# Kernel tuning notes

Hardware: AMD Instinct MI355X
Metric: run time of the kernel (lower is better)

## Reference

```python
import jax, jax.numpy as jnp
from jax import lax
import numpy as np

# Vim-tiny config
D_MODEL, D_INNER, D_STATE, DT_RANK, K_CONV, DEPTH = 192, 384, 16, 12, 4, 24
BATCH, IMG, PATCH = 8, 224, 16
L = (IMG // PATCH) ** 2  # 196 tokens
EPS = 1e-5


def setup_inputs() -> dict:
    key = jax.random.key(0)
    ks = jax.random.split(key, 12)
    std = 0.02
    x = jax.random.normal(ks[0], (BATCH, 3, IMG, IMG), jnp.float32)
    patch_w = jax.random.normal(ks[1], (D_MODEL, 3, PATCH, PATCH), jnp.float32) * std
    patch_b = jnp.zeros((D_MODEL,), jnp.float32)
    norm_w = jnp.ones((DEPTH, D_MODEL), jnp.float32)
    norm_b = jnp.zeros((DEPTH, D_MODEL), jnp.float32)
    in_proj_w = jax.random.normal(ks[2], (DEPTH, 2 * D_INNER, D_MODEL), jnp.float32) * std
    conv_w = jax.random.normal(ks[3], (DEPTH, D_INNER, K_CONV), jnp.float32) * 0.2
    conv_b = jnp.zeros((DEPTH, D_INNER), jnp.float32)
    x_proj_w = jax.random.normal(ks[4], (DEPTH, DT_RANK + 2 * D_STATE, D_INNER), jnp.float32) * std
    dt_proj_w = jax.random.normal(ks[5], (DEPTH, D_INNER, DT_RANK), jnp.float32) * std
    # softplus^{-1}(0.01): standard mamba dt init
    dt_proj_b = jnp.full((DEPTH, D_INNER), float(np.log(np.expm1(0.01))), jnp.float32)
    # S4D-real init: A = -[1..d_state]
    A_log = jnp.broadcast_to(jnp.log(jnp.arange(1, D_STATE + 1, dtype=jnp.float32)),
                             (DEPTH, D_INNER, D_STATE)).copy()
    D_param = jnp.ones((DEPTH, D_INNER), jnp.float32)
    out_proj_w = jax.random.normal(ks[6], (DEPTH, D_MODEL, D_INNER), jnp.float32) * std
    normf_w = jnp.ones((D_MODEL,), jnp.float32)
    normf_b = jnp.zeros((D_MODEL,), jnp.float32)
    return dict(x=x, patch_w=patch_w, patch_b=patch_b, norm_w=norm_w, norm_b=norm_b,
                in_proj_w=in_proj_w, conv_w=conv_w, conv_b=conv_b, x_proj_w=x_proj_w,
                dt_proj_w=dt_proj_w, dt_proj_b=dt_proj_b, A_log=A_log, D_param=D_param,
                out_proj_w=out_proj_w, normf_w=normf_w, normf_b=normf_b)


def layernorm(h, w, b):
    mu = jnp.mean(h, axis=-1, keepdims=True)
    var = jnp.mean(jnp.square(h - mu), axis=-1, keepdims=True)
    return (h - mu) * lax.rsqrt(var + EPS) * w + b


def mamba_mixer(h, ipw, cw, cb, xpw, dtw, dtb, a_log, d_p, opw):
    # h: [B, L, d_model]
    xz = jnp.einsum('bld,ed->ble', h, ipw)          # [B, L, 2*d_inner]
    xi, z = jnp.split(xz, 2, axis=-1)
    # depthwise causal conv1d (left pad k-1, keep first L outputs)
    xt = xi.transpose(0, 2, 1)                       # [B, d_inner, L]
    xc = lax.conv_general_dilated(xt, cw[:, None, :], (1,), [(K_CONV - 1, 0)],
                                  dimension_numbers=('NCH', 'OIH', 'NCH'),
                                  feature_group_count=D_INNER) + cb[None, :, None]
    xc = jax.nn.silu(xc).transpose(0, 2, 1)          # [B, L, d_inner]
    dbl = jnp.einsum('bld,ed->ble', xc, xpw)         # [B, L, dt_rank+2*d_state]
    dt = jax.nn.softplus(jnp.einsum('blr,dr->bld', dbl[..., :DT_RANK], dtw) + dtb)
    Bm = dbl[..., DT_RANK:DT_RANK + D_STATE]         # [B, L, d_state]
    Cm = dbl[..., DT_RANK + D_STATE:]                # [B, L, d_state]
    A = -jnp.exp(a_log)                              # [d_inner, d_state]
    dA = jnp.exp(dt[..., None] * A)                  # [B, L, d_inner, d_state]
    dBx = (dt * xc)[..., None] * Bm[:, :, None, :]   # [B, L, d_inner, d_state]

    def step(hst, inp):
        a, bx, c = inp
        hst = a * hst + bx
        return hst, jnp.einsum('bds,bs->bd', hst, c)

    h0 = jnp.zeros((h.shape[0], D_INNER, D_STATE), h.dtype)
    _, ys = lax.scan(step, h0, (dA.transpose(1, 0, 2, 3), dBx.transpose(1, 0, 2, 3),
                                Cm.transpose(1, 0, 2)))
    y = ys.transpose(1, 0, 2) + d_p * xc             # [B, L, d_inner]
    y = y * jax.nn.silu(z)
    return jnp.einsum('ble,de->bld', y, opw)


def reference(x, patch_w, patch_b, norm_w, norm_b, in_proj_w, conv_w, conv_b,
              x_proj_w, dt_proj_w, dt_proj_b, A_log, D_param, out_proj_w,
              normf_w, normf_b):
    # patch embedding: strided conv then flatten HW -> tokens
    emb = lax.conv_general_dilated(x, patch_w, (PATCH, PATCH), 'VALID',
                                   dimension_numbers=('NCHW', 'OIHW', 'NCHW'))
    emb = emb + patch_b[None, :, None, None]
    b = emb.shape[0]
    hidden = emb.reshape(b, D_MODEL, -1).transpose(0, 2, 1)   # [B, L, d_model]
    residual = jnp.zeros_like(hidden)

    def layer_step(carry, p):
        h, res = carry
        nw, nb, ipw, cw, cb, xpw, dtw, dtb, al, dp, opw = p
        res = res + h
        h = layernorm(res, nw, nb)
        h = mamba_mixer(h, ipw, cw, cb, xpw, dtw, dtb, al, dp, opw)
        return (h, res), None

    (hidden, residual), _ = lax.scan(
        layer_step, (hidden, residual),
        (norm_w, norm_b, in_proj_w, conv_w, conv_b, x_proj_w,
         dt_proj_w, dt_proj_b, A_log, D_param, out_proj_w))
    residual = residual + hidden
    return layernorm(residual, normf_w, normf_b)     # [B, L, d_model]
```

## Files before the change

kernel.cpp:

```cpp
#include <hip/hip_runtime.h>

#define NROWS 1568
#define MPAD  1600
#define LSEQ  196
#define EPS   1e-5f
#define TCH   7
#define NCH   28

typedef __attribute__((ext_vector_type(8))) short short8_t;
typedef __attribute__((ext_vector_type(8))) unsigned short ush8;
typedef __attribute__((ext_vector_type(4))) float f32x4;
typedef unsigned short ush;

__device__ __forceinline__ float silu_(float x) { return x / (1.f + expf(-x)); }
__device__ __forceinline__ float fsilu_(float x) { return x / (1.f + __expf(-x)); }

__device__ __forceinline__ ush bfh_(float f) {
  unsigned u = __float_as_uint(f);
  return (ush)((u + 0x7FFFu + ((u >> 16) & 1u)) >> 16);
}
__device__ __forceinline__ float bf2f_(ush h) {
  return __uint_as_float(((unsigned)h) << 16);
}

__device__ __forceinline__ void glds16(const ush* g, ush* l) {
  __builtin_amdgcn_global_load_lds(
      (const __attribute__((address_space(1))) void*)g,
      (__attribute__((address_space(3))) void*)l, 16, 0, 0);
}

#define N8_PW  18432
#define N8_IPW 442368
#define N8_OPW 221184
__global__ __launch_bounds__(256) void wsplit3_k(const float* __restrict__ pw,
                                                 const float* __restrict__ ipw,
                                                 const float* __restrict__ opw,
                                                 ush* __restrict__ pw_h, ush* __restrict__ pw_l,
                                                 ush* __restrict__ ipw_h, ush* __restrict__ ipw_l,
                                                 ush* __restrict__ opw_h, ush* __restrict__ opw_l) {
  int i = blockIdx.x * 256 + threadIdx.x;
  const float* src;
  ush *hi, *lo;
  size_t off;
  if (i < N8_PW) { src = pw; hi = pw_h; lo = pw_l; off = i; }
  else if (i < N8_PW + N8_IPW) { src = ipw; hi = ipw_h; lo = ipw_l; off = i - N8_PW; }
  else if (i < N8_PW + N8_IPW + N8_OPW) { src = opw; hi = opw_h; lo = opw_l; off = i - N8_PW - N8_IPW; }
  else return;
  float v[8];
  *(float4*)&v[0] = *(const float4*)(src + off * 8);
  *(float4*)&v[4] = *(const float4*)(src + off * 8 + 4);
  ush8 h8, l8;
#pragma unroll
  for (int j = 0; j < 8; ++j) {
    ush h = bfh_(v[j]);
    h8[j] = h;
    l8[j] = bfh_(v[j] - bf2f_(h));
  }
  *(ush8*)&hi[off * 8] = h8;
  *(ush8*)&lo[off * 8] = l8;
}

__global__ __launch_bounds__(256) void zeros_k(float* __restrict__ res,
                                               ush* __restrict__ a_h, ush* __restrict__ a_l,
                                               ush* __restrict__ hn_h, ush* __restrict__ hn_l,
                                               ush* __restrict__ y_h, ush* __restrict__ y_l) {
  int i = blockIdx.x * 256 + threadIdx.x;
  ush8 z = {};
  if (i < 75264) ((float4*)res)[i] = float4{0.f, 0.f, 0.f, 0.f};
  if (i < 3072) {
    ((ush8*)(a_h + (size_t)NROWS * 768))[i] = z;
    ((ush8*)(a_l + (size_t)NROWS * 768))[i] = z;
  }
  if (i < 768) {
    ((ush8*)(hn_h + (size_t)NROWS * 192))[i] = z;
    ((ush8*)(hn_l + (size_t)NROWS * 192))[i] = z;
  }
  if (i < 1536) {
    ((ush8*)(y_h + (size_t)NROWS * 384))[i] = z;
    ((ush8*)(y_l + (size_t)NROWS * 384))[i] = z;
  }
}

__global__ __launch_bounds__(256) void im2col_k(const float* __restrict__ x,
                                                ush* __restrict__ Ah,
                                                ush* __restrict__ Al) {
  int i8 = blockIdx.x * 256 + threadIdx.x;
  if (i8 >= NROWS * 768 / 8) return;
  int idx = i8 * 8;
  int m = idx / 768, r = idx - m * 768;
  int b = m / LSEQ, l = m - b * LSEQ;
  int ph = l / 14, pw = l - ph * 14;
  int c = r >> 8, rem = r & 255, ii = rem >> 4, j = rem & 15;
  const float* src = &x[((b * 3 + c) * 224 + ph * 16 + ii) * 224 + pw * 16 + j];
  float v[8];
  *(float4*)&v[0] = *(const float4*)&src[0];
  *(float4*)&v[4] = *(const float4*)&src[4];
  ush8 h8, l8;
#pragma unroll
  for (int k = 0; k < 8; ++k) {
    ush h = bfh_(v[k]);
    h8[k] = h;
    l8[k] = bfh_(v[k] - bf2f_(h));
  }
  *(ush8*)&Ah[idx] = h8;
  *(ush8*)&Al[idx] = l8;
}

__global__ __launch_bounds__(256) void gemm64g_k(const ush* __restrict__ Ah_g,
                                                 const ush* __restrict__ Al_g,
                                                 const ush* __restrict__ Wh_g,
                                                 const ush* __restrict__ Wl_g,
                                                 const float* __restrict__ bias,
                                                 float* __restrict__ C, int N, int K) {
  __shared__ ush sAh[3][2048], sAl[3][2048], sWh[3][2048], sWl[3][2048];
  const int tid = threadIdx.x, lane = tid & 63, wave = tid >> 6;
  const int ntiles = N / 64;
  const int row0 = (blockIdx.x / ntiles) * 64, col0 = (blockIdx.x % ntiles) * 64;
  const int sr = wave * 16 + (lane >> 2);
  const int j8 = ((lane & 3) ^ ((sr >> 1) & 3)) * 8;
  const size_t gaA = (size_t)(row0 + sr) * K + j8;
  const size_t gaW = (size_t)(col0 + sr) * K + j8;
  const int lb = wave * 512;
  const int nsteps = K >> 5;

  glds16(Ah_g + gaA, &sAh[0][lb]);
  glds16(Al_g + gaA, &sAl[0][lb]);
  glds16(Wh_g + gaW, &sWh[0][lb]);
  glds16(Wl_g + gaW, &sWl[0][lb]);
  glds16(Ah_g + gaA + 32, &sAh[1][lb]);
  glds16(Al_g + gaA + 32, &sAl[1][lb]);
  glds16(Wh_g + gaW + 32, &sWh[1][lb]);
  glds16(Wl_g + gaW + 32, &sWl[1][lb]);

  const int fr = lane & 15, fg = lane >> 4;
  const int wm = (wave & 1) * 32, wn = (wave >> 1) * 32;
  f32x4 acc[2][2] = {};
  int cur = 0;

  for (int s = 0; s < nsteps; ++s) {
    if (s < nsteps - 1) asm volatile("s_waitcnt vmcnt(4)" ::: "memory");
    else                asm volatile("s_waitcnt vmcnt(0)" ::: "memory");
    __builtin_amdgcn_s_barrier();
    __builtin_amdgcn_sched_barrier(0);
    if (s + 2 < nsteps) {
      int nk = (s + 2) * 32;
      int nb = (cur >= 1) ? cur - 1 : 2;
      glds16(Ah_g + gaA + nk, &sAh[nb][lb]);
      glds16(Al_g + gaA + nk, &sAl[nb][lb]);
      glds16(Wh_g + gaW + nk, &sWh[nb][lb]);
      glds16(Wl_g + gaW + nk, &sWl[nb][lb]);
    }
    short8_t ah[2], al[2], wh[2], wl[2];
#pragma unroll
    for (int i = 0; i < 2; ++i) {
      int ra = wm + i * 16 + fr;
      int oa = ra * 32 + ((fg ^ ((ra >> 1) & 3)) << 3);
      ah[i] = *(short8_t*)&sAh[cur][oa];
      al[i] = *(short8_t*)&sAl[cur][oa];
      int rw = wn + i * 16 + fr;
      int ow = rw * 32 + ((fg ^ ((rw >> 1) & 3)) << 3);
      wh[i] = *(short8_t*)&sWh[cur][ow];
      wl[i] = *(short8_t*)&sWl[cur][ow];
    }
#pragma unroll
    for (int i = 0; i < 2; ++i)
#pragma unroll
      for (int j = 0; j < 2; ++j) {
        acc[i][j] = __builtin_amdgcn_mfma_f32_16x16x32_bf16(ah[i], wh[j], acc[i][j], 0, 0, 0);
        acc[i][j] = __builtin_amdgcn_mfma_f32_16x16x32_bf16(ah[i], wl[j], acc[i][j], 0, 0, 0);
        acc[i][j] = __builtin_amdgcn_mfma_f32_16x16x32_bf16(al[i], wh[j], acc[i][j], 0, 0, 0);
      }
    cur = (cur == 2) ? 0 : cur + 1;
  }

#pragma unroll
  for (int i = 0; i < 2; ++i)
#pragma unroll
    for (int j = 0; j < 2; ++j)
#pragma unroll
      for (int r = 0; r < 4; ++r) {
        int m = row0 + wm + i * 16 + fg * 4 + r;
        int n = col0 + wn + j * 16 + fr;
        float o = acc[i][j][r];
        if (bias) o += bias[n];
        C[(size_t)m * N + n] = o;
      }
}

__global__ __launch_bounds__(256) void gemm32g_k(const ush* __restrict__ Ah_g,
                                                 const ush* __restrict__ Al_g,
                                                 const ush* __restrict__ Wh_g,
                                                 const ush* __restrict__ Wl_g,
                                                 float* __restrict__ C, int N, int K) {
  __shared__ ush sAh[3][1024], sAl[3][1024], sWh[3][1024], sWl[3][1024];
  const int tid = threadIdx.x, lane = tid & 63, wave = tid >> 6;
  const int ntiles = N / 32;
  const int row0 = (blockIdx.x / ntiles) * 32, col0 = (blockIdx.x % ntiles) * 32;
  const int sr = (wave & 1) * 16 + (lane >> 2);
  const int j8 = ((lane & 3) ^ ((sr >> 1) & 3)) * 8;
  const bool isA = wave < 2;
  const size_t ga = (size_t)((isA ? row0 : col0) + sr) * K + j8;
  const ush* gh = isA ? Ah_g : Wh_g;
  const ush* gl = isA ? Al_g : Wl_g;
  const int lb = (wave & 1) * 512;
  const int nsteps = K >> 5;

  {
    ush* dh0 = isA ? &sAh[0][lb] : &sWh[0][lb];
    ush* dl0 = isA ? &sAl[0][lb] : &sWl[0][lb];
    glds16(gh + ga, dh0);
    glds16(gl + ga, dl0);
    ush* dh1 = isA ? &sAh[1][lb] : &sWh[1][lb];
    ush* dl1 = isA ? &sAl[1][lb] : &sWl[1][lb];
    glds16(gh + ga + 32, dh1);
    glds16(gl + ga + 32, dl1);
  }

  const int fr = lane & 15, fg = lane >> 4;
  const int wrow = wave & 1, wcol = wave >> 1;
  f32x4 acc = {};
  int cur = 0;

  for (int s = 0; s < nsteps; ++s) {
    if (s < nsteps - 1) asm volatile("s_waitcnt vmcnt(2)" ::: "memory");
    else                asm volatile("s_waitcnt vmcnt(0)" ::: "memory");
    __builtin_amdgcn_s_barrier();
    __builtin_amdgcn_sched_barrier(0);
    if (s + 2 < nsteps) {
      int nk = (s + 2) * 32;
      int nb = (cur >= 1) ? cur - 1 : 2;
      ush* dh = isA ? &sAh[nb][lb] : &sWh[nb][lb];
      ush* dl = isA ? &sAl[nb][lb] : &sWl[nb][lb];
      glds16(gh + ga + nk, dh);
      glds16(gl + ga + nk, dl);
    }
    int ra = wrow * 16 + fr;
    int oa = ra * 32 + ((fg ^ ((ra >> 1) & 3)) << 3);
    short8_t ah = *(short8_t*)&sAh[cur][oa];
    short8_t al = *(short8_t*)&sAl[cur][oa];
    int rw = wcol * 16 + fr;
    int ow = rw * 32 + ((fg ^ ((rw >> 1) & 3)) << 3);
    short8_t wh = *(short8_t*)&sWh[cur][ow];
    short8_t wl = *(short8_t*)&sWl[cur][ow];
    acc = __builtin_amdgcn_mfma_f32_16x16x32_bf16(ah, wh, acc, 0, 0, 0);
    acc = __builtin_amdgcn_mfma_f32_16x16x32_bf16(ah, wl, acc, 0, 0, 0);
    acc = __builtin_amdgcn_mfma_f32_16x16x32_bf16(al, wh, acc, 0, 0, 0);
    cur = (cur == 2) ? 0 : cur + 1;
  }

#pragma unroll
  for (int r = 0; r < 4; ++r) {
    int m = row0 + wrow * 16 + fg * 4 + r;
    int n = col0 + wcol * 16 + fr;
    C[(size_t)m * N + n] = acc[r];
  }
}

__global__ __launch_bounds__(256) void addlnbf_k(float* __restrict__ res,
                                                 const float* __restrict__ h,
                                                 const float* __restrict__ w,
                                                 const float* __restrict__ b,
                                                 ush* __restrict__ out_h,
                                                 ush* __restrict__ out_l) {
  int n = blockIdx.x * 4 + (threadIdx.x >> 6);
  int t = threadIdx.x & 63;
  float v[3];
  float s = 0.f;
#pragma unroll
  for (int i = 0; i < 3; ++i) {
    int d = t + 64 * i;
    float r = res[(size_t)n * 192 + d] + h[(size_t)n * 192 + d];
    res[(size_t)n * 192 + d] = r;
    v[i] = r;
    s += r;
  }
#pragma unroll
  for (int off = 32; off >= 1; off >>= 1) s += __shfl_xor(s, off);
  float mu = s * (1.f / 192.f);
  float q = 0.f;
#pragma unroll
  for (int i = 0; i < 3; ++i) { float dd = v[i] - mu; q += dd * dd; }
#pragma unroll
  for (int off = 32; off >= 1; off >>= 1) q += __shfl_xor(q, off);
  float inv = rsqrtf(q * (1.f / 192.f) + EPS);
#pragma unroll
  for (int i = 0; i < 3; ++i) {
    int d = t + 64 * i;
    float o = (v[i] - mu) * inv * w[d] + b[d];
    ush hh = bfh_(o);
    out_h[(size_t)n * 192 + d] = hh;
    out_l[(size_t)n * 192 + d] = bfh_(o - bf2f_(hh));
  }
}

__global__ __launch_bounds__(256) void lnfin_k(const float* __restrict__ res,
                                               const float* __restrict__ h,
                                               const float* __restrict__ w,
                                               const float* __restrict__ b,
                                               float* __restrict__ out) {
  int n = blockIdx.x * 4 + (threadIdx.x >> 6);
  int lane = threadIdx.x & 63;
  if (n >= NROWS) return;
  float v[3];
  float s = 0.f;
#pragma unroll
  for (int i = 0; i < 3; ++i) {
    int d = lane + 64 * i;
    float r = res[(size_t)n * 192 + d] + h[(size_t)n * 192 + d];
    v[i] = r;
    s += r;
  }
#pragma unroll
  for (int off = 32; off >= 1; off >>= 1) s += __shfl_xor(s, off);
  float mu = s * (1.f / 192.f);
  float q = 0.f;
#pragma unroll
  for (int i = 0; i < 3; ++i) { float dd = v[i] - mu; q += dd * dd; }
#pragma unroll
  for (int off = 32; off >= 1; off >>= 1) q += __shfl_xor(q, off);
  float inv = rsqrtf(q * (1.f / 192.f) + EPS);
#pragma unroll
  for (int i = 0; i < 3; ++i) {
    int d = lane + 64 * i;
    out[(size_t)n * 192 + d] = (v[i] - mu) * inv * w[d] + b[d];
  }
}

__global__ __launch_bounds__(384) void conv4_k(const float* __restrict__ xz,
                                               const float* __restrict__ cw,
                                               const float* __restrict__ cb,
                                               const float* __restrict__ xpw,
                                               const float* __restrict__ dtw,
                                               const float* __restrict__ dtb,
                                               const float* __restrict__ dpar,
                                               float* __restrict__ dbl,
                                               float* __restrict__ pk) {
  __shared__ __align__(16) float xcl[4][384];
  __shared__ __align__(16) float dbll[4][48];
  const int t = threadIdx.x;
  const int n0 = blockIdx.x * 4;
  const int l0 = n0 % LSEQ;

  float cwv[4];
  *(float4*)cwv = *(const float4*)(cw + t * 4);
  float cbv = cb[t];
#pragma unroll
  for (int r = 0; r < 4; ++r) {
    int l = l0 + r, n = n0 + r;
    float acc = cbv;
#pragma unroll
    for (int k = 0; k < 4; ++k) {
      int ll = l - 3 + k;
      if (ll >= 0) acc += xz[(size_t)(n - 3 + k) * 768 + t] * cwv[k];
    }
    float v = fsilu_(acc);
    xcl[r][t] = v;
  }
  __syncthreads();

  if (t < 352) {
    const int e = t >> 3, part = t & 7;
    const float4* w4 = (const float4*)(xpw + e * 384 + part * 48);
    const float4* x0 = (const float4*)(&xcl[0][part * 48]);
    const float4* x1 = (const float4*)(&xcl[1][part * 48]);
    const float4* x2 = (const float4*)(&xcl[2][part * 48]);
    const float4* x3 = (const float4*)(&xcl[3][part * 48]);
    float s0 = 0.f, s1 = 0.f, s2 = 0.f, s3 = 0.f;
#pragma unroll
    for (int k = 0; k < 12; ++k) {
      float4 w = w4[k], a;
      a = x0[k]; s0 += a.x * w.x + a.y * w.y + a.z * w.z + a.w * w.w;
      a = x1[k]; s1 += a.x * w.x + a.y * w.y + a.z * w.z + a.w * w.w;
      a = x2[k]; s2 += a.x * w.x + a.y * w.y + a.z * w.z + a.w * w.w;
      a = x3[k]; s3 += a.x * w.x + a.y * w.y + a.z * w.z + a.w * w.w;
    }
#pragma unroll
    for (int off = 1; off <= 4; off <<= 1) {
      s0 += __shfl_xor(s0, off);
      s1 += __shfl_xor(s1, off);
      s2 += __shfl_xor(s2, off);
      s3 += __shfl_xor(s3, off);
    }
    if (part == 0) {
      dbll[0][e] = s0; dbl[(size_t)(n0 + 0) * 44 + e] = s0;
      dbll[1][e] = s1; dbl[(size_t)(n0 + 1) * 44 + e] = s1;
      dbll[2][e] = s2; dbl[(size_t)(n0 + 2) * 44 + e] = s2;
      dbll[3][e] = s3; dbl[(size_t)(n0 + 3) * 44 + e] = s3;
    }
  }
  __syncthreads();

  const float4* dw4 = (const float4*)(dtw + t * 12);
  float4 dw0 = dw4[0], dw1 = dw4[1], dw2 = dw4[2];
  float dtbv = dtb[t];
  float Dp = dpar[t];
#pragma unroll
  for (int r = 0; r < 4; ++r) {
    int n = n0 + r;
    const float4* bb = (const float4*)(&dbll[r][0]);
    float4 b0 = bb[0], b1 = bb[1], b2 = bb[2];
    float a = dtbv
            + dw0.x * b0.x + dw0.y * b0.y + dw0.z * b0.z + dw0.w * b0.w
            + dw1.x * b1.x + dw1.y * b1.y + dw1.z * b1.z + dw1.w * b1.w
            + dw2.x * b2.x + dw2.y * b2.y + dw2.z * b2.z + dw2.w * b2.w;
    float sp = fmaxf(a, 0.f) + __logf(1.f + __expf(-fabsf(a)));
    float xcv = xcl[r][t];
    float zv = xz[(size_t)n * 768 + 384 + t];
    float gz = fsilu_(zv);
    *(float4*)&pk[((size_t)n * 384 + t) * 4] = float4{sp, sp * xcv, Dp * xcv, gz};
  }
}

__global__ __launch_bounds__(448) void scanF_k(const float* __restrict__ pk,
                                               const float* __restrict__ dbl,
                                               const float* __restrict__ a_log,
                                               ush* __restrict__ y_h,
                                               ush* __restrict__ y_l) {
  __shared__ float Pl[4][NCH][17];
  __shared__ float Sl[4][NCH][17];
  const int t = threadIdx.x;
  const int p = t / 112;
  const int r = t - p * 112;
  const int c = r >> 2, e = r & 3;
  const int s4 = e * 4;
  const int bd = blockIdx.x * 4 + p;
  const int b = bd / 384, d = bd - b * 384;
  float A[4];
#pragma unroll
  for (int j = 0; j < 4; ++j) A[j] = -expf(a_log[d * 16 + s4 + j]);

  float e_c[TCH], g_c[TCH], q_c[TCH][4];
  float h[4] = {0.f, 0.f, 0.f, 0.f};
  float pr[4] = {1.f, 1.f, 1.f, 1.f};
  const int base = b * LSEQ + c * TCH;

#pragma unroll
  for (int i = 0; i < TCH; ++i) {
    int n = base + i;
    float4 pkv = *(const float4*)&pk[((size_t)n * 384 + d) * 4];
    float4 Bv = *(const float4*)&dbl[(size_t)n * 44 + 12 + s4];
    float4 Cv = *(const float4*)&dbl[(size_t)n * 44 + 28 + s4];
    float a0 = __expf(pkv.x * A[0]);
    float a1 = __expf(pkv.x * A[1]);
    float a2 = __expf(pkv.x * A[2]);
    float a3 = __expf(pkv.x * A[3]);
    h[0] = a0 * h[0] + pkv.y * Bv.x; pr[0] *= a0;
    h[1] = a1 * h[1] + pkv.y * Bv.y; pr[1] *= a1;
    h[2] = a2 * h[2] + pkv.y * Bv.z; pr[2] *= a2;
    h[3] = a3 * h[3] + pkv.y * Bv.w; pr[3] *= a3;
    float psl = h[0] * Cv.x + h[1] * Cv.y + h[2] * Cv.z + h[3] * Cv.w;
    psl += __shfl_xor(psl, 1);
    psl += __shfl_xor(psl, 2);
    e_c[i] = (psl + pkv.z) * pkv.w;
    g_c[i] = pkv.w;
    q_c[i][0] = pr[0] * Cv.x;
    q_c[i][1] = pr[1] * Cv.y;
    q_c[i][2] = pr[2] * Cv.z;
    q_c[i][3] = pr[3] * Cv.w;
  }
#pragma unroll
  for (int j = 0; j < 4; ++j) {
    Pl[p][c][s4 + j] = pr[j];
    Sl[p][c][s4 + j] = h[j];
  }
  __syncthreads();

  if (t < 64) {
    int pp = t >> 4, ss = t & 15;
    float S_run = Sl[pp][0][ss];
    for (int cc = 1; cc < NCH; ++cc) {
      S_run = Pl[pp][cc][ss] * S_run + Sl[pp][cc][ss];
      Sl[pp][cc][ss] = S_run;
    }
  }
  __syncthreads();

  float h0[4] = {0.f, 0.f, 0.f, 0.f};
  if (c > 0) {
#pragma unroll
    for (int j = 0; j < 4; ++j) h0[j] = Sl[p][c - 1][s4 + j];
  }
#pragma unroll
  for (int i = 0; i < TCH; ++i) {
    float corr = h0[0] * q_c[i][0] + h0[1] * q_c[i][1]
               + h0[2] * q_c[i][2] + h0[3] * q_c[i][3];
    corr += __shfl_xor(corr, 1);
    corr += __shfl_xor(corr, 2);
    if (e == 0) {
      int n = base + i;
      float o = e_c[i] + corr * g_c[i];
      ush hh = bfh_(o);
      y_h[(size_t)n * 384 + d] = hh;
      y_l[(size_t)n * 384 + d] = bfh_(o - bf2f_(hh));
    }
  }
}

extern "C" void kernel_launch(void* const* d_in, const int* in_sizes, int n_in,
                              void* d_out, int out_size, void* d_ws, size_t ws_size,
                              hipStream_t stream) {
  const float* x        = (const float*)d_in[0];
  const float* patch_w  = (const float*)d_in[1];
  const float* patch_b  = (const float*)d_in[2];
  const float* norm_w   = (const float*)d_in[3];
  const float* norm_b   = (const float*)d_in[4];
  const float* in_proj_w  = (const float*)d_in[5];
  const float* conv_w   = (const float*)d_in[6];
  const float* conv_b   = (const float*)d_in[7];
  const float* x_proj_w = (const float*)d_in[8];
  const float* dt_proj_w = (const float*)d_in[9];
  const float* dt_proj_b = (const float*)d_in[10];
  const float* A_log    = (const float*)d_in[11];
  const float* D_param  = (const float*)d_in[12];
  const float* out_proj_w = (const float*)d_in[13];
  const float* normf_w  = (const float*)d_in[14];
  const float* normf_b  = (const float*)d_in[15];
  float* out = (float*)d_out;
  float* ws = (float*)d_ws;

  float* res = ws;
  float* xz  = ws + 301056;
  float* dbl = ws + 1529856;
  float* h   = ws + 1598848;
  float* pk  = ws + 1906048;
  ush* ub = (ush*)(ws + 4314496);
  ush* a_h  = ub;
  ush* a_l  = ub + 1228800;
  ush* hn_h = ub + 2457600;
  ush* hn_l = ub + 2764800;
  ush* y_h  = ub + 3072000;
  ush* y_l  = ub + 3686400;
  ush* pw_h = ub + 4300800;
  ush* pw_l = ub + 4448256;
  ush* ipw_h = ub + 4595712;
  ush* ipw_l = ub + 8134656;
  ush* opw_h = ub + 11673600;
  ush* opw_l = ub + 13443072;

  zeros_k<<<294, 256, 0, stream>>>(res, a_h, a_l, hn_h, hn_l, y_h, y_l);
  wsplit3_k<<<(N8_PW + N8_IPW + N8_OPW + 255) / 256, 256, 0, stream>>>(
      patch_w, in_proj_w, out_proj_w, pw_h, pw_l, ipw_h, ipw_l, opw_h, opw_l);
  im2col_k<<<(NROWS * 768 / 8 + 255) / 256, 256, 0, stream>>>(x, a_h, a_l);
  gemm64g_k<<<75, 256, 0, stream>>>(a_h, a_l, pw_h, pw_l, patch_b, h, 192, 768);

  for (int L = 0; L < 24; ++L) {
    addlnbf_k<<<NROWS / 4, 256, 0, stream>>>(res, h, norm_w + L * 192, norm_b + L * 192, hn_h, hn_l);
    gemm64g_k<<<300, 256, 0, stream>>>(hn_h, hn_l,
        ipw_h + (size_t)L * 147456, ipw_l + (size_t)L * 147456, nullptr, xz, 768, 192);
    conv4_k<<<NROWS / 4, 384, 0, stream>>>(xz,
        conv_w + (size_t)L * 1536, conv_b + (size_t)L * 384,
        x_proj_w + (size_t)L * 16896,
        dt_proj_w + (size_t)L * 4608, dt_proj_b + (size_t)L * 384,
        D_param + (size_t)L * 384, dbl, pk);
    scanF_k<<<768, 448, 0, stream>>>(pk, dbl,
        A_log + (size_t)L * 6144, y_h, y_l);
    gemm32g_k<<<300, 256, 0, stream>>>(y_h, y_l,
        opw_h + (size_t)L * 73728, opw_l + (size_t)L * 73728, h, 192, 384);
  }

  lnfin_k<<<392, 256, 0, stream>>>(res, h, normf_w, normf_b, out);
}
```

Baseline: 1.068 ms.

## Fuse residual add and layernorm into the in_proj GEMM prologue

Removes the separate add+layernorm kernel and the hn bf16 split buffers by computing the residual add, layernorm and bf16 hi/lo split inside a new in_proj GEMM kernel that keeps the normalized A tile in shared memory. The residual is ping-ponged between two buffers so that only column-tile 0 writes the updated residual while the other blocks read the old one. This saves one launch per layer and the round trip of the normalized activations, at the cost of recomputing the layernorm in all 12 column tiles and using a 32x64 tile layout with 600 blocks.

```diff
diff --git a/kernel.cpp b/kernel.cpp
--- a/kernel.cpp
+++ b/kernel.cpp
@@ -62,18 +62,13 @@
 
 __global__ __launch_bounds__(256) void zeros_k(float* __restrict__ res,
                                                ush* __restrict__ a_h, ush* __restrict__ a_l,
-                                               ush* __restrict__ hn_h, ush* __restrict__ hn_l,
                                                ush* __restrict__ y_h, ush* __restrict__ y_l) {
   int i = blockIdx.x * 256 + threadIdx.x;
   ush8 z = {};
-  if (i < 75264) ((float4*)res)[i] = float4{0.f, 0.f, 0.f, 0.f};
+  if (i < 76800) ((float4*)res)[i] = float4{0.f, 0.f, 0.f, 0.f};
   if (i < 3072) {
     ((ush8*)(a_h + (size_t)NROWS * 768))[i] = z;
     ((ush8*)(a_l + (size_t)NROWS * 768))[i] = z;
-  }
-  if (i < 768) {
-    ((ush8*)(hn_h + (size_t)NROWS * 192))[i] = z;
-    ((ush8*)(hn_l + (size_t)NROWS * 192))[i] = z;
   }
   if (i < 1536) {
     ((ush8*)(y_h + (size_t)NROWS * 384))[i] = z;
@@ -185,6 +180,128 @@
         if (bias) o += bias[n];
         C[(size_t)m * N + n] = o;
       }
+}
+
+__global__ __launch_bounds__(256) void gemm_inln_k(const float* __restrict__ res_in,
+                                                   float* __restrict__ res_out,
+                                                   const float* __restrict__ hprev,
+                                                   const float* __restrict__ lnw,
+                                                   const float* __restrict__ lnb,
+                                                   const ush* __restrict__ Wh_g,
+                                                   const ush* __restrict__ Wl_g,
+                                                   float* __restrict__ C) {
+  __shared__ float sA[6400];
+  __shared__ ush sWh[3][2048], sWl[3][2048];
+  ush* sAh = (ush*)sA;
+  ush* sAl = sAh + 6400;
+  const int tid = threadIdx.x, lane = tid & 63, wave = tid >> 6;
+  const int t = blockIdx.x;
+  const int rt = t / 12, ct = t - rt * 12;
+  const int row0 = rt * 32, col0 = ct * 64;
+
+  const int sr = wave * 16 + (lane >> 2);
+  const int j8 = ((lane & 3) ^ ((sr >> 1) & 3)) * 8;
+  const size_t gaW = (size_t)(col0 + sr) * 192 + j8;
+  const int lb = wave * 512;
+  glds16(Wh_g + gaW, &sWh[0][lb]);
+  glds16(Wl_g + gaW, &sWl[0][lb]);
+  glds16(Wh_g + gaW + 32, &sWh[1][lb]);
+  glds16(Wl_g + gaW + 32, &sWl[1][lb]);
+
+#pragma unroll
+  for (int i = 0; i < 6; ++i) {
+    int idx = tid + i * 256;
+    int row = idx / 48, c4 = idx - row * 48;
+    size_t g = (size_t)(row0 + row) * 192 + c4 * 4;
+    float4 a = *(const float4*)&res_in[g];
+    float4 b = *(const float4*)&hprev[g];
+    float4 r{a.x + b.x, a.y + b.y, a.z + b.z, a.w + b.w};
+    *(float4*)&sA[row * 192 + c4 * 4] = r;
+    if (ct == 0) *(float4*)&res_out[g] = r;
+  }
+  __syncthreads();
+
+  float o[8][3];
+#pragma unroll
+  for (int rr = 0; rr < 8; ++rr) {
+    int row = wave * 8 + rr;
+    float v0 = sA[row * 192 + lane];
+    float v1 = sA[row * 192 + lane + 64];
+    float v2 = sA[row * 192 + lane + 128];
+    float s = v0 + v1 + v2;
+#pragma unroll
+    for (int off = 32; off >= 1; off >>= 1) s += __shfl_xor(s, off);
+    float mu = s * (1.f / 192.f);
+    float d0 = v0 - mu, d1 = v1 - mu, d2 = v2 - mu;
+    float q = d0 * d0 + d1 * d1 + d2 * d2;
+#pragma unroll
+    for (int off = 32; off >= 1; off >>= 1) q += __shfl_xor(q, off);
+    float inv = rsqrtf(q * (1.f / 192.f) + EPS);
+    o[rr][0] = d0 * inv * lnw[lane] + lnb[lane];
+    o[rr][1] = d1 * inv * lnw[lane + 64] + lnb[lane + 64];
+    o[rr][2] = d2 * inv * lnw[lane + 128] + lnb[lane + 128];
+  }
+  __syncthreads();
+
+#pragma unroll
+  for (int rr = 0; rr < 8; ++rr) {
+    int row = wave * 8 + rr;
+    int swr = (row >> 1) & 3;
+#pragma unroll
+    for (int i = 0; i < 3; ++i) {
+      int c = lane + 64 * i;
+      int sc = (c & ~31) | ((((c >> 3) & 3) ^ swr) << 3) | (c & 7);
+      float x = o[rr][i];
+      ush hh = bfh_(x);
+      sAh[row * 200 + sc] = hh;
+      sAl[row * 200 + sc] = bfh_(x - bf2f_(hh));
+    }
+  }
+  __syncthreads();
+
+  const int fr = lane & 15, fg = lane >> 4;
+  const int wrow = wave & 1, wcol = wave >> 1;
+  f32x4 acc[2] = {};
+  int cur = 0;
+  for (int s = 0; s < 6; ++s) {
+    if (s > 0) {
+      if (s < 5) asm volatile("s_waitcnt vmcnt(2)" ::: "memory");
+      else       asm volatile("s_waitcnt vmcnt(0)" ::: "memory");
+      __builtin_amdgcn_s_barrier();
+      __builtin_amdgcn_sched_barrier(0);
+    }
+    if (s + 2 < 6) {
+      int nk = (s + 2) * 32;
+      int nb = (s + 2) % 3;
+      glds16(Wh_g + gaW + nk, &sWh[nb][lb]);
+      glds16(Wl_g + gaW + nk, &sWl[nb][lb]);
+    }
+    int kk = s * 32;
+    int ra = wrow * 16 + fr;
+    int oa = ra * 200 + kk + ((fg ^ ((ra >> 1) & 3)) << 3);
+    short8_t ah = *(short8_t*)&sAh[oa];
+    short8_t al = *(short8_t*)&sAl[oa];
+#pragma unroll
+    for (int jt = 0; jt < 2; ++jt) {
+      int rw = wcol * 32 + jt * 16 + fr;
+      int ow = rw * 32 + ((fg ^ ((rw >> 1) & 3)) << 3);
+      short8_t wh = *(short8_t*)&sWh[cur][ow];
+      short8_t wl = *(short8_t*)&sWl[cur][ow];
+      acc[jt] = __builtin_amdgcn_mfma_f32_16x16x32_bf16(ah, wh, acc[jt], 0, 0, 0);
+      acc[jt] = __builtin_amdgcn_mfma_f32_16x16x32_bf16(ah, wl, acc[jt], 0, 0, 0);
+      acc[jt] = __builtin_amdgcn_mfma_f32_16x16x32_bf16(al, wh, acc[jt], 0, 0, 0);
+    }
+    cur = (cur == 2) ? 0 : cur + 1;
+  }
+
+#pragma unroll
+  for (int jt = 0; jt < 2; ++jt)
+#pragma unroll
+    for (int r = 0; r < 4; ++r) {
+      int m = row0 + wrow * 16 + fg * 4 + r;
+      int n = col0 + wcol * 32 + jt * 16 + fr;
+      C[(size_t)m * 768 + n] = acc[jt][r];
+    }
 }
 
 __global__ __launch_bounds__(256) void gemm32g_k(const ush* __restrict__ Ah_g,
@@ -253,43 +370,6 @@
     int m = row0 + wrow * 16 + fg * 4 + r;
     int n = col0 + wcol * 16 + fr;
     C[(size_t)m * N + n] = acc[r];
-  }
-}
-
-__global__ __launch_bounds__(256) void addlnbf_k(float* __restrict__ res,
-                                                 const float* __restrict__ h,
-                                                 const float* __restrict__ w,
-                                                 const float* __restrict__ b,
-                                                 ush* __restrict__ out_h,
-                                                 ush* __restrict__ out_l) {
-  int n = blockIdx.x * 4 + (threadIdx.x >> 6);
-  int t = threadIdx.x & 63;
-  float v[3];
-  float s = 0.f;
-#pragma unroll
-  for (int i = 0; i < 3; ++i) {
-    int d = t + 64 * i;
-    float r = res[(size_t)n * 192 + d] + h[(size_t)n * 192 + d];
-    res[(size_t)n * 192 + d] = r;
-    v[i] = r;
-    s += r;
-  }
-#pragma unroll
-  for (int off = 32; off >= 1; off >>= 1) s += __shfl_xor(s, off);
-  float mu = s * (1.f / 192.f);
-  float q = 0.f;
-#pragma unroll
-  for (int i = 0; i < 3; ++i) { float dd = v[i] - mu; q += dd * dd; }
-#pragma unroll
-  for (int off = 32; off >= 1; off >>= 1) q += __shfl_xor(q, off);
-  float inv = rsqrtf(q * (1.f / 192.f) + EPS);
-#pragma unroll
-  for (int i = 0; i < 3; ++i) {
-    int d = t + 64 * i;
-    float o = (v[i] - mu) * inv * w[d] + b[d];
-    ush hh = bfh_(o);
-    out_h[(size_t)n * 192 + d] = hh;
-    out_l[(size_t)n * 192 + d] = bfh_(o - bf2f_(hh));
   }
 }
 
@@ -518,35 +598,36 @@
   float* out = (float*)d_out;
   float* ws = (float*)d_ws;
 
-  float* res = ws;
-  float* xz  = ws + 301056;
-  float* dbl = ws + 1529856;
-  float* h   = ws + 1598848;
-  float* pk  = ws + 1906048;
-  ush* ub = (ush*)(ws + 4314496);
+  float* resA = ws;
+  float* resB = ws + 307200;
+  float* xz   = ws + 614400;
+  float* dbl  = ws + 1843200;
+  float* h    = ws + 1912192;
+  float* pk   = ws + 2219392;
+  ush* ub = (ush*)(ws + 4627840);
   ush* a_h  = ub;
   ush* a_l  = ub + 1228800;
-  ush* hn_h = ub + 2457600;
-  ush* hn_l = ub + 2764800;
-  ush* y_h  = ub + 3072000;
-  ush* y_l  = ub + 3686400;
-  ush* pw_h = ub + 4300800;
-  ush* pw_l = ub + 4448256;
-  ush* ipw_h = ub + 4595712;
-  ush* ipw_l = ub + 8134656;
-  ush* opw_h = ub + 11673600;
-  ush* opw_l = ub + 13443072;
-
-  zeros_k<<<294, 256, 0, stream>>>(res, a_h, a_l, hn_h, hn_l, y_h, y_l);
+  ush* y_h  = ub + 2457600;
+  ush* y_l  = ub + 3072000;
+  ush* pw_h = ub + 3686400;
+  ush* pw_l = ub + 3833856;
+  ush* ipw_h = ub + 3981312;
+  ush* ipw_l = ub + 7520256;
+  ush* opw_h = ub + 11059200;
+  ush* opw_l = ub + 12828672;
+
+  zeros_k<<<300, 256, 0, stream>>>(resA, a_h, a_l, y_h, y_l);
   wsplit3_k<<<(N8_PW + N8_IPW + N8_OPW + 255) / 256, 256, 0, stream>>>(
       patch_w, in_proj_w, out_proj_w, pw_h, pw_l, ipw_h, ipw_l, opw_h, opw_l);
   im2col_k<<<(NROWS * 768 / 8 + 255) / 256, 256, 0, stream>>>(x, a_h, a_l);
   gemm64g_k<<<75, 256, 0, stream>>>(a_h, a_l, pw_h, pw_l, patch_b, h, 192, 768);
 
   for (int L = 0; L < 24; ++L) {
-    addlnbf_k<<<NROWS / 4, 256, 0, stream>>>(res, h, norm_w + L * 192, norm_b + L * 192, hn_h, hn_l);
-    gemm64g_k<<<300, 256, 0, stream>>>(hn_h, hn_l,
-        ipw_h + (size_t)L * 147456, ipw_l + (size_t)L * 147456, nullptr, xz, 768, 192);
+    const float* rin = (L & 1) ? resB : resA;
+    float* rout = (L & 1) ? resA : resB;
+    gemm_inln_k<<<600, 256, 0, stream>>>(rin, rout, h,
+        norm_w + L * 192, norm_b + L * 192,
+        ipw_h + (size_t)L * 147456, ipw_l + (size_t)L * 147456, xz);
     conv4_k<<<NROWS / 4, 384, 0, stream>>>(xz,
         conv_w + (size_t)L * 1536, conv_b + (size_t)L * 384,
         x_proj_w + (size_t)L * 16896,
@@ -558,5 +639,5 @@
         opw_h + (size_t)L * 73728, opw_l + (size_t)L * 73728, h, 192, 384);
   }
 
-  lnfin_k<<<392, 256, 0, stream>>>(res, h, normf_w, normf_b, out);
-}
+  lnfin_k<<<392, 256, 0, stream>>>(resA, h, normf_w, normf_b, out);
+}
```

Measured after the change: 1.148 ms. +7.4%, slower.
